# Optimization experiments

Hardware: AMD Instinct MI355X
Metric: run time of the kernel (lower is better)

Reference implementation:

```python
import jax, jax.numpy as jnp
import numpy as np

NEG_SLOPE = 0.2


def gat_conv(x, edge_index, W, a_src, a_dst, b, concat):
    """PyG-style GATConv: add self-loops, linear, edge attention, scatter-softmax, scatter-add."""
    N = x.shape[0]
    H, C = a_src.shape
    loop = jnp.arange(N)
    src = jnp.concatenate([edge_index[0], loop])  # source j (messages flow j -> i)
    dst = jnp.concatenate([edge_index[1], loop])  # target i (aggregation node)
    h = (x @ W).reshape(N, H, C)                  # [N,H,C]
    alpha_s = jnp.sum(h * a_src, axis=-1)         # [N,H]
    alpha_d = jnp.sum(h * a_dst, axis=-1)         # [N,H]
    e = jax.nn.leaky_relu(alpha_s[src] + alpha_d[dst], NEG_SLOPE)  # [E,H]
    # numerically stable scatter-softmax over edges grouped by destination node
    m = jax.ops.segment_max(e, dst, num_segments=N)                # [N,H]
    ex = jnp.exp(e - m[dst])
    denom = jax.ops.segment_sum(ex, dst, num_segments=N)           # [N,H]
    alpha = ex / (denom[dst] + 1e-16)                              # [E,H]
    out = jax.ops.segment_sum(h[src] * alpha[:, :, None], dst, num_segments=N)  # [N,H,C]
    out = out.reshape(N, H * C) if concat else out.mean(axis=1)
    return out + b


def setup_inputs() -> dict:
    key = jax.random.key(0)
    ks = jax.random.split(key, 12)
    N, E, F_IN, HID, OUT, HEADS = 100000, 1600000, 128, 128, 64, 4
    C1 = HID // HEADS
    x = jax.random.normal(ks[0], (N, F_IN), dtype=jnp.float32)
    edge_index = jax.random.randint(ks[1], (2, E), 0, N, dtype=jnp.int64)
    s = 0.05
    return {
        "x": x,
        "edge_index": edge_index,
        "W1": jax.random.normal(ks[2], (F_IN, HEADS * C1), dtype=jnp.float32) * s,
        "a_src1": jax.random.normal(ks[3], (HEADS, C1), dtype=jnp.float32) * s,
        "a_dst1": jax.random.normal(ks[4], (HEADS, C1), dtype=jnp.float32) * s,
        "b1": jnp.zeros((HEADS * C1,), dtype=jnp.float32),
        "W2": jax.random.normal(ks[5], (HID, OUT), dtype=jnp.float32) * s,
        "a_src2": jax.random.normal(ks[6], (1, OUT), dtype=jnp.float32) * s,
        "a_dst2": jax.random.normal(ks[7], (1, OUT), dtype=jnp.float32) * s,
        "b2": jnp.zeros((OUT,), dtype=jnp.float32),
    }


def reference(x, edge_index, W1, a_src1, a_dst1, b1, W2, a_src2, a_dst2, b2):
    h = jax.nn.elu(gat_conv(x, edge_index, W1, a_src1, a_dst1, b1, concat=True))
    # F.dropout(p=0.5, training=False) is the identity in eval mode
    out = gat_conv(h, edge_index, W2, a_src2, a_dst2, b2, concat=False)
    return out
```

## Files before the change

kernel.cpp:

```cpp
#include <hip/hip_runtime.h>
#include <hip/hip_fp16.h>
#include <math.h>
#include <string.h>


#define BSH 9
#define DPB 512
#define NBK 256
#define CH1 16384
#define LOG2E 1.44269504088896f

__device__ __forceinline__ float exp2_fast(float x) {
#if __has_builtin(__builtin_amdgcn_exp2f)
    return __builtin_amdgcn_exp2f(x);
#else
    return exp2f(x);
#endif
}


__global__ __launch_bounds__(256) void bucket_hist(const int* __restrict__ ei, int E, int N,
                                                   unsigned* __restrict__ bcount) {
    __shared__ unsigned hist[NBK];
    int t = threadIdx.x;
    hist[t] = 0;
    __syncthreads();
    int Etot = E + N;
    for (int k = blockIdx.x * 256 + t; k < Etot; k += gridDim.x * 256) {
        int d = (k < E) ? ei[E + k] : (k - E);
        atomicAdd(&hist[d >> BSH], 1u);
    }
    __syncthreads();
    unsigned c = hist[t];
    if (c) atomicAdd(&bcount[t], c);
}

__global__ void scan_buckets(const unsigned* __restrict__ bcount, unsigned* __restrict__ bbase,
                             unsigned* __restrict__ bcursor) {
    __shared__ unsigned s[NBK];
    int t = threadIdx.x;
    unsigned v = bcount[t];
    s[t] = v;
    __syncthreads();
    for (int o = 1; o < NBK; o <<= 1) {
        unsigned add = (t >= o) ? s[t - o] : 0;
        __syncthreads();
        s[t] += add;
        __syncthreads();
    }
    unsigned excl = s[t] - v;
    bbase[t] = excl;
    bcursor[t] = excl;
    if (t == NBK - 1) bbase[NBK] = excl + v;
}

__global__ __launch_bounds__(256) void bucket_scatter(const int* __restrict__ ei, int E, int N,
                                                      unsigned* __restrict__ bcursor,
                                                      unsigned* __restrict__ rec) {
    __shared__ unsigned hist[NBK];
    __shared__ unsigned base[NBK];
    int t = threadIdx.x;
    hist[t] = 0;
    __syncthreads();
    int Etot = E + N;
    int k0 = blockIdx.x * CH1;
    int k1 = min(k0 + CH1, Etot);
    for (int k = k0 + t; k < k1; k += 256) {
        int d = (k < E) ? ei[E + k] : (k - E);
        atomicAdd(&hist[d >> BSH], 1u);
    }
    __syncthreads();
    unsigned c = hist[t];
    base[t] = c ? atomicAdd(&bcursor[t], c) : 0u;
    hist[t] = 0;
    __syncthreads();
    for (int k = k0 + t; k < k1; k += 256) {
        int s, d;
        if (k < E) { s = ei[k]; d = ei[E + k]; } else { s = d = k - E; }
        int b = d >> BSH;
        unsigned r = atomicAdd(&hist[b], 1u);
        rec[base[b] + r] = (unsigned)s | ((unsigned)(d & (DPB - 1)) << 17);
    }
}

__global__ __launch_bounds__(256) void bucket_sort(const unsigned* __restrict__ rec,
                                                   const unsigned* __restrict__ bbase,
                                                   int* __restrict__ offs, int* __restrict__ srcs,
                                                   int N, int Etot) {
    __shared__ unsigned hist[DPB];
    __shared__ unsigned tsum[256];
    int t = threadIdx.x, bb = blockIdx.x;
    unsigned r0 = bbase[bb], r1 = bbase[bb + 1];
    hist[t] = 0;
    hist[t + 256] = 0;
    __syncthreads();
    int dlo = bb << BSH;
    for (unsigned k = r0 + t; k < r1; k += 256) {
        unsigned e = rec[k];
        atomicAdd(&hist[e >> 17], 1u);
    }
    __syncthreads();
    unsigned h0 = hist[2 * t], h1 = hist[2 * t + 1];
    tsum[t] = h0 + h1;
    __syncthreads();
    for (int o = 1; o < 256; o <<= 1) {
        unsigned a = (t >= o) ? tsum[t - o] : 0;
        __syncthreads();
        tsum[t] += a;
        __syncthreads();
    }
    unsigned tb = tsum[t] - (h0 + h1);
    int d0 = dlo + 2 * t;
    if (d0 < N) offs[d0] = (int)(r0 + tb);
    if (d0 + 1 < N) offs[d0 + 1] = (int)(r0 + tb + h0);
    hist[2 * t] = tb;
    hist[2 * t + 1] = tb + h0;
    __syncthreads();
    for (unsigned k = r0 + t; k < r1; k += 256) {
        unsigned e = rec[k];
        unsigned r = atomicAdd(&hist[e >> 17], 1u);
        srcs[r0 + r] = (int)(e & 0x1FFFFu);
    }
    if (bb == 0 && t == 0) offs[N] = Etot;
}


template <int NC, int H, typename InT, typename OutT>
__global__ __launch_bounds__(256) void gemm_k128(const InT* __restrict__ A,
                                                 const float* __restrict__ B,
                                                 OutT* __restrict__ C,
                                                 const float* __restrict__ a_src,
                                                 const float* __restrict__ a_dst,
                                                 float* __restrict__ as,
                                                 float* __restrict__ ad, int M) {
    constexpr int BM = 64, BK = 32, K = 128;
    constexpr int TPR = NC / 4;
    constexpr int R = BM / (256 / TPR);
    constexpr int TXH = TPR / H;
    __shared__ float AsT[BK][BM + 4];
    __shared__ float Bs[BK][NC];
    int tid = threadIdx.x;
    int tx = tid % TPR, ty = tid / TPR;
    int rowBase = blockIdx.x * BM;
    float acc[R][4] = {};
    for (int k0 = 0; k0 < K; k0 += BK) {
#pragma unroll
        for (int i = 0; i < 4; ++i) {
            int lin = tid + i * 256;
            int row = lin >> 4;
            int kp = lin & 15;
            int grow = rowBase + row;
            if (grow >= M) grow = M - 1;
            float2 v;
            if constexpr (sizeof(InT) == 2) {
                __half2 hv = *reinterpret_cast<const __half2*>((const __half*)A + (size_t)grow * K + k0 + kp * 2);
                v = __half22float2(hv);
            } else {
                v = *reinterpret_cast<const float2*>((const float*)A + (size_t)grow * K + k0 + kp * 2);
            }
            AsT[kp * 2][row] = v.x;
            AsT[kp * 2 + 1][row] = v.y;
        }
#pragma unroll
        for (int i = 0; i < (BK * NC) / 1024; ++i) {
            int lin = tid + i * 256;
            int row = lin / (NC / 4);
            int col4 = lin % (NC / 4);
            float4 v = *reinterpret_cast<const float4*>(B + (size_t)(k0 + row) * NC + col4 * 4);
            *reinterpret_cast<float4*>(&Bs[row][col4 * 4]) = v;
        }
        __syncthreads();
#pragma unroll
        for (int kk = 0; kk < BK; ++kk) {
            float4 bv = *reinterpret_cast<const float4*>(&Bs[kk][tx * 4]);
            float a[R];
#pragma unroll
            for (int r4 = 0; r4 < R; r4 += 4) {
                float4 av = *reinterpret_cast<const float4*>(&AsT[kk][ty * R + r4]);
                a[r4] = av.x; a[r4 + 1] = av.y; a[r4 + 2] = av.z; a[r4 + 3] = av.w;
            }
#pragma unroll
            for (int r = 0; r < R; ++r) {
                acc[r][0] = fmaf(a[r], bv.x, acc[r][0]);
                acc[r][1] = fmaf(a[r], bv.y, acc[r][1]);
                acc[r][2] = fmaf(a[r], bv.z, acc[r][2]);
                acc[r][3] = fmaf(a[r], bv.w, acc[r][3]);
            }
        }
        __syncthreads();
    }
    float4 asv = *reinterpret_cast<const float4*>(a_src + tx * 4);
    float4 adv = *reinterpret_cast<const float4*>(a_dst + tx * 4);
#pragma unroll
    for (int r = 0; r < R; ++r) {
        int grow = rowBase + ty * R + r;
        bool live = grow < M;
        if (live) {
            if constexpr (sizeof(OutT) == 2) {
                __half2 p0 = __floats2half2_rn(acc[r][0], acc[r][1]);
                __half2 p1 = __floats2half2_rn(acc[r][2], acc[r][3]);
                __half2* cp = reinterpret_cast<__half2*>((__half*)C + (size_t)grow * NC + tx * 4);
                cp[0] = p0;
                cp[1] = p1;
            } else {
                float4 v = make_float4(acc[r][0], acc[r][1], acc[r][2], acc[r][3]);
                *reinterpret_cast<float4*>((float*)C + (size_t)grow * NC + tx * 4) = v;
            }
        }
        float ps = acc[r][0] * asv.x + acc[r][1] * asv.y + acc[r][2] * asv.z + acc[r][3] * asv.w;
        float pd = acc[r][0] * adv.x + acc[r][1] * adv.y + acc[r][2] * adv.z + acc[r][3] * adv.w;
#pragma unroll
        for (int o = 1; o < TXH; o <<= 1) {
            ps += __shfl_xor(ps, o, 64);
            pd += __shfl_xor(pd, o, 64);
        }
        if ((tx & (TXH - 1)) == 0 && live) {
            int head = tx / TXH;
            as[(size_t)grow * H + head] = ps * LOG2E;
            ad[(size_t)grow * H + head] = pd * LOG2E;
        }
    }
}


template <int H, int ROWS, int COFF, int CW, bool DOELU, typename OutT>
__global__ __launch_bounds__(256) void aggregateQ(const __half* __restrict__ h,
                                                  const float* __restrict__ as,
                                                  const float* __restrict__ ad,
                                                  const int* __restrict__ offs,
                                                  const int* __restrict__ srcs,
                                                  const float* __restrict__ bias,
                                                  OutT* __restrict__ out, int N) {
    constexpr int CPL = CW / 16;
    constexpr int NH2 = CPL / 2;
    unsigned wave = (blockIdx.x * blockDim.x + threadIdx.x) >> 6;
    unsigned lane = threadIdx.x & 63;
    unsigned lig = lane & 15;
    unsigned node = wave * 4u + (lane >> 4);
    bool live = node < (unsigned)N;
    unsigned nc = live ? node : (unsigned)(N - 1);
    unsigned chan = COFF + lig * CPL;
    unsigned head = (chan * H) / ROWS;
    float adv = ad[nc * H + head];
    int e0 = offs[nc], e1 = offs[nc + 1];
    int deg = e1 - e0, e1m1 = e1 - 1;
    int md = deg;
    md = max(md, __shfl_xor(md, 16, 64));
    md = max(md, __shfl_xor(md, 32, 64));
    float2 acc[NH2] = {};
    float den = 0.f;
    for (int k = 0; k < md; k += 2) {
        unsigned ja = (unsigned)srcs[min(e0 + k, e1m1)];
        unsigned jb = (unsigned)srcs[min(e0 + k + 1, e1m1)];
        float ta = as[ja * H + head] + adv;
        float tb = as[jb * H + head] + adv;
        __half2 ha[NH2], hb[NH2];
        if constexpr (NH2 == 4) {
            uint4 va = *reinterpret_cast<const uint4*>(h + ja * (unsigned)ROWS + chan);
            uint4 vb = *reinterpret_cast<const uint4*>(h + jb * (unsigned)ROWS + chan);
            memcpy(ha, &va, 16);
            memcpy(hb, &vb, 16);
        } else {
            uint2 va = *reinterpret_cast<const uint2*>(h + ja * (unsigned)ROWS + chan);
            uint2 vb = *reinterpret_cast<const uint2*>(h + jb * (unsigned)ROWS + chan);
            memcpy(ha, &va, 8);
            memcpy(hb, &vb, 8);
        }
        float xa = exp2_fast(fmaxf(ta, 0.2f * ta));
        float xb = exp2_fast(fmaxf(tb, 0.2f * tb));
        xa = (k < deg) ? xa : 0.f;
        xb = (k + 1 < deg) ? xb : 0.f;
#pragma unroll
        for (int q = 0; q < NH2; ++q) {
            float2 fa = __half22float2(ha[q]);
            float2 fb = __half22float2(hb[q]);
            acc[q].x = fmaf(xa, fa.x, acc[q].x);
            acc[q].y = fmaf(xa, fa.y, acc[q].y);
            acc[q].x = fmaf(xb, fb.x, acc[q].x);
            acc[q].y = fmaf(xb, fb.y, acc[q].y);
        }
        den += xa + xb;
    }
    float r = 1.0f / (den + 1e-16f);
    if (!live) return;
    const float* bp = bias + chan;
    if constexpr (sizeof(OutT) == 2) {
        __half2 st[NH2];
#pragma unroll
        for (int q = 0; q < NH2; ++q) {
            float v0 = acc[q].x * r + bp[2 * q];
            float v1 = acc[q].y * r + bp[2 * q + 1];
            if constexpr (DOELU) {
                v0 = (v0 > 0.f) ? v0 : expm1f(v0);
                v1 = (v1 > 0.f) ? v1 : expm1f(v1);
            }
            st[q] = __floats2half2_rn(v0, v1);
        }
        if constexpr (NH2 == 4) {
            uint4 v; memcpy(&v, st, 16);
            *reinterpret_cast<uint4*>((__half*)out + node * (unsigned)ROWS + chan) = v;
        } else {
            uint2 v; memcpy(&v, st, 8);
            *reinterpret_cast<uint2*>((__half*)out + node * (unsigned)ROWS + chan) = v;
        }
    } else {
        float vs[CPL];
#pragma unroll
        for (int q = 0; q < NH2; ++q) {
            float v0 = acc[q].x * r + bp[2 * q];
            float v1 = acc[q].y * r + bp[2 * q + 1];
            if constexpr (DOELU) {
                v0 = (v0 > 0.f) ? v0 : expm1f(v0);
                v1 = (v1 > 0.f) ? v1 : expm1f(v1);
            }
            vs[2 * q] = v0;
            vs[2 * q + 1] = v1;
        }
#pragma unroll
        for (int q4 = 0; q4 < CPL; q4 += 4) {
            float4 v = make_float4(vs[q4], vs[q4 + 1], vs[q4 + 2], vs[q4 + 3]);
            *reinterpret_cast<float4*>((float*)out + node * (unsigned)ROWS + chan + q4) = v;
        }
    }
}


extern "C" void kernel_launch(void* const* d_in, const int* in_sizes, int n_in,
                              void* d_out, int out_size, void* d_ws, size_t ws_size,
                              hipStream_t stream) {
    const float* x      = (const float*)d_in[0];
    const int*   ei     = (const int*)d_in[1];
    const float* W1     = (const float*)d_in[2];
    const float* a_src1 = (const float*)d_in[3];
    const float* a_dst1 = (const float*)d_in[4];
    const float* b1     = (const float*)d_in[5];
    const float* W2     = (const float*)d_in[6];
    const float* a_src2 = (const float*)d_in[7];
    const float* a_dst2 = (const float*)d_in[8];
    const float* b2     = (const float*)d_in[9];
    float* out = (float*)d_out;

    const int N = out_size / 64;
    const int E = in_sizes[1] / 2;
    const int Etot = E + N;

    size_t off = 0;
    auto carve = [&](size_t bytes) -> void* {
        void* p = (char*)d_ws + off;
        off += (bytes + 255) & ~(size_t)255;
        return p;
    };
    __half* h1      = (__half*)carve((size_t)N * 128 * 2);
    __half* hmid    = (__half*)carve((size_t)N * 128 * 2);
    float* as1      = (float*)carve((size_t)N * 4 * 4);
    float* ad1      = (float*)carve((size_t)N * 4 * 4);
    float* as2      = (float*)carve((size_t)N * 4);
    float* ad2      = (float*)carve((size_t)N * 4);
    int*   offs     = (int*)carve((size_t)(N + 1) * 4);
    int*   srcs     = (int*)carve((size_t)Etot * 4);
    unsigned* rec   = (unsigned*)carve((size_t)Etot * 4);
    unsigned* bcount  = (unsigned*)carve(NBK * 4);
    unsigned* bbase   = (unsigned*)carve((NBK + 1) * 4);
    unsigned* bcursor = (unsigned*)carve(NBK * 4);
    __half* h2      = h1;

    hipMemsetAsync(bcount, 0, NBK * sizeof(unsigned), stream);
    bucket_hist<<<128, 256, 0, stream>>>(ei, E, N, bcount);
    scan_buckets<<<1, 256, 0, stream>>>(bcount, bbase, bcursor);
    bucket_scatter<<<(Etot + CH1 - 1) / CH1, 256, 0, stream>>>(ei, E, N, bcursor, rec);
    bucket_sort<<<(N + DPB - 1) / DPB, 256, 0, stream>>>(rec, bbase, offs, srcs, N, Etot);

    gemm_k128<128, 4, float, __half><<<(N + 63) / 64, 256, 0, stream>>>(
        x, W1, h1, a_src1, a_dst1, as1, ad1, N);
    aggregateQ<4, 128, 0, 64, true, __half><<<(N + 15) / 16, 256, 0, stream>>>(
        h1, as1, ad1, offs, srcs, b1, hmid, N);
    aggregateQ<4, 128, 64, 64, true, __half><<<(N + 15) / 16, 256, 0, stream>>>(
        h1, as1, ad1, offs, srcs, b1, hmid, N);

    gemm_k128<64, 1, __half, __half><<<(N + 63) / 64, 256, 0, stream>>>(
        hmid, W2, h2, a_src2, a_dst2, as2, ad2, N);
    aggregateQ<1, 64, 0, 64, false, float><<<(N + 15) / 16, 256, 0, stream>>>(
        h2, as2, ad2, offs, srcs, b2, out, N);
}
```

Before: 416.0 us.

## Use MFMA f16 matrix cores for GEMMs and merge split layer-1 aggregation

Replaces the scalar-FMA shared-memory GEMM with a kernel built on mfma_f32_16x16x32_f16. The weights are first transposed and cast to half, and the attention projections are computed from the accumulator fragments with lane shuffles. It also merges the two half-channel layer-1 aggregation launches into one launch covering all 128 channels. Inputs and weights now enter the GEMM as fp16, which lowers precision compared with the fp32 FMA path. The per-element stores of C are scattered 2-byte writes, which may cost bandwidth.

```diff
diff --git a/kernel.cpp b/kernel.cpp
--- a/kernel.cpp
+++ b/kernel.cpp
@@ -9,6 +9,9 @@
 #define NBK 256
 #define CH1 16384
 #define LOG2E 1.44269504088896f
+
+using half8 = __attribute__((ext_vector_type(8))) _Float16;
+using floatx4 = __attribute__((ext_vector_type(4))) float;
 
 __device__ __forceinline__ float exp2_fast(float x) {
 #if __has_builtin(__builtin_amdgcn_exp2f)
@@ -125,105 +128,93 @@
 }
 
 
-template <int NC, int H, typename InT, typename OutT>
-__global__ __launch_bounds__(256) void gemm_k128(const InT* __restrict__ A,
-                                                 const float* __restrict__ B,
-                                                 OutT* __restrict__ C,
+__global__ void transpose_w(const float* __restrict__ W, __half* __restrict__ Wt,
+                            int K, int Nc) {
+    int idx = blockIdx.x * 256 + threadIdx.x;
+    if (idx >= K * Nc) return;
+    int n = idx / K, k = idx - n * K;
+    Wt[n * K + k] = __float2half(W[k * Nc + n]);
+}
+
+
+template <int NC, int H, typename InT>
+__global__ __launch_bounds__(256) void gemm_mfma(const InT* __restrict__ A,
+                                                 const __half* __restrict__ Wt,
+                                                 __half* __restrict__ C,
                                                  const float* __restrict__ a_src,
                                                  const float* __restrict__ a_dst,
                                                  float* __restrict__ as,
                                                  float* __restrict__ ad, int M) {
-    constexpr int BM = 64, BK = 32, K = 128;
-    constexpr int TPR = NC / 4;
-    constexpr int R = BM / (256 / TPR);
-    constexpr int TXH = TPR / H;
-    __shared__ float AsT[BK][BM + 4];
-    __shared__ float Bs[BK][NC];
-    int tid = threadIdx.x;
-    int tx = tid % TPR, ty = tid / TPR;
-    int rowBase = blockIdx.x * BM;
-    float acc[R][4] = {};
-    for (int k0 = 0; k0 < K; k0 += BK) {
-#pragma unroll
-        for (int i = 0; i < 4; ++i) {
-            int lin = tid + i * 256;
-            int row = lin >> 4;
-            int kp = lin & 15;
-            int grow = rowBase + row;
-            if (grow >= M) grow = M - 1;
-            float2 v;
-            if constexpr (sizeof(InT) == 2) {
-                __half2 hv = *reinterpret_cast<const __half2*>((const __half*)A + (size_t)grow * K + k0 + kp * 2);
-                v = __half22float2(hv);
-            } else {
-                v = *reinterpret_cast<const float2*>((const float*)A + (size_t)grow * K + k0 + kp * 2);
-            }
-            AsT[kp * 2][row] = v.x;
-            AsT[kp * 2 + 1][row] = v.y;
-        }
-#pragma unroll
-        for (int i = 0; i < (BK * NC) / 1024; ++i) {
-            int lin = tid + i * 256;
-            int row = lin / (NC / 4);
-            int col4 = lin % (NC / 4);
-            float4 v = *reinterpret_cast<const float4*>(B + (size_t)(k0 + row) * NC + col4 * 4);
-            *reinterpret_cast<float4*>(&Bs[row][col4 * 4]) = v;
-        }
-        __syncthreads();
-#pragma unroll
-        for (int kk = 0; kk < BK; ++kk) {
-            float4 bv = *reinterpret_cast<const float4*>(&Bs[kk][tx * 4]);
-            float a[R];
-#pragma unroll
-            for (int r4 = 0; r4 < R; r4 += 4) {
-                float4 av = *reinterpret_cast<const float4*>(&AsT[kk][ty * R + r4]);
-                a[r4] = av.x; a[r4 + 1] = av.y; a[r4 + 2] = av.z; a[r4 + 3] = av.w;
-            }
-#pragma unroll
-            for (int r = 0; r < R; ++r) {
-                acc[r][0] = fmaf(a[r], bv.x, acc[r][0]);
-                acc[r][1] = fmaf(a[r], bv.y, acc[r][1]);
-                acc[r][2] = fmaf(a[r], bv.z, acc[r][2]);
-                acc[r][3] = fmaf(a[r], bv.w, acc[r][3]);
-            }
-        }
-        __syncthreads();
-    }
-    float4 asv = *reinterpret_cast<const float4*>(a_src + tx * 4);
-    float4 adv = *reinterpret_cast<const float4*>(a_dst + tx * 4);
-#pragma unroll
-    for (int r = 0; r < R; ++r) {
-        int grow = rowBase + ty * R + r;
-        bool live = grow < M;
+    constexpr int NT = NC / 16;
+    constexpr int TPH = NT / H;
+    int wave = threadIdx.x >> 6;
+    int lane = threadIdx.x & 63;
+    int quad = lane >> 4, col = lane & 15;
+    int row0 = blockIdx.x * 64 + wave * 16;
+    int arow = row0 + col;
+    if (arow >= M) arow = M - 1;
+    floatx4 acc[NT] = {};
+    const __half* wp = Wt + col * 128 + quad * 8;
+#pragma unroll
+    for (int k0 = 0; k0 < 128; k0 += 32) {
+        half8 af;
+        if constexpr (sizeof(InT) == 4) {
+            const float* ap = (const float*)A + (size_t)arow * 128 + k0 + quad * 8;
+            float4 v0 = *reinterpret_cast<const float4*>(ap);
+            float4 v1 = *reinterpret_cast<const float4*>(ap + 4);
+            af[0] = (_Float16)v0.x; af[1] = (_Float16)v0.y;
+            af[2] = (_Float16)v0.z; af[3] = (_Float16)v0.w;
+            af[4] = (_Float16)v1.x; af[5] = (_Float16)v1.y;
+            af[6] = (_Float16)v1.z; af[7] = (_Float16)v1.w;
+        } else {
+            af = *reinterpret_cast<const half8*>((const __half*)A + (size_t)arow * 128 + k0 + quad * 8);
+        }
+#pragma unroll
+        for (int t = 0; t < NT; ++t) {
+            half8 bf = *reinterpret_cast<const half8*>(wp + t * 16 * 128 + k0);
+            acc[t] = __builtin_amdgcn_mfma_f32_16x16x32_f16(af, bf, acc[t], 0, 0, 0);
+        }
+    }
+    float sa[NT], da[NT];
+#pragma unroll
+    for (int t = 0; t < NT; ++t) {
+        sa[t] = a_src[t * 16 + col];
+        da[t] = a_dst[t * 16 + col];
+    }
+    int rbase = row0 + quad * 4;
+#pragma unroll
+    for (int reg = 0; reg < 4; ++reg) {
+        int row = rbase + reg;
+        bool live = row < M;
         if (live) {
-            if constexpr (sizeof(OutT) == 2) {
-                __half2 p0 = __floats2half2_rn(acc[r][0], acc[r][1]);
-                __half2 p1 = __floats2half2_rn(acc[r][2], acc[r][3]);
-                __half2* cp = reinterpret_cast<__half2*>((__half*)C + (size_t)grow * NC + tx * 4);
-                cp[0] = p0;
-                cp[1] = p1;
-            } else {
-                float4 v = make_float4(acc[r][0], acc[r][1], acc[r][2], acc[r][3]);
-                *reinterpret_cast<float4*>((float*)C + (size_t)grow * NC + tx * 4) = v;
-            }
-        }
-        float ps = acc[r][0] * asv.x + acc[r][1] * asv.y + acc[r][2] * asv.z + acc[r][3] * asv.w;
-        float pd = acc[r][0] * adv.x + acc[r][1] * adv.y + acc[r][2] * adv.z + acc[r][3] * adv.w;
-#pragma unroll
-        for (int o = 1; o < TXH; o <<= 1) {
-            ps += __shfl_xor(ps, o, 64);
-            pd += __shfl_xor(pd, o, 64);
-        }
-        if ((tx & (TXH - 1)) == 0 && live) {
-            int head = tx / TXH;
-            as[(size_t)grow * H + head] = ps * LOG2E;
-            ad[(size_t)grow * H + head] = pd * LOG2E;
-        }
-    }
-}
-
-
-template <int H, int ROWS, int COFF, int CW, bool DOELU, typename OutT>
+#pragma unroll
+            for (int t = 0; t < NT; ++t)
+                C[(size_t)row * NC + t * 16 + col] = __float2half(acc[t][reg]);
+        }
+#pragma unroll
+        for (int h = 0; h < H; ++h) {
+            float ps = 0.f, pd = 0.f;
+#pragma unroll
+            for (int tt = 0; tt < TPH; ++tt) {
+                int t = h * TPH + tt;
+                ps = fmaf(acc[t][reg], sa[t], ps);
+                pd = fmaf(acc[t][reg], da[t], pd);
+            }
+#pragma unroll
+            for (int o = 1; o < 16; o <<= 1) {
+                ps += __shfl_xor(ps, o, 64);
+                pd += __shfl_xor(pd, o, 64);
+            }
+            if (col == 0 && live) {
+                as[(size_t)row * H + h] = ps * LOG2E;
+                ad[(size_t)row * H + h] = pd * LOG2E;
+            }
+        }
+    }
+}
+
+
+template <int H, int ROWS, int CW, bool DOELU, typename OutT>
 __global__ __launch_bounds__(256) void aggregateQ(const __half* __restrict__ h,
                                                   const float* __restrict__ as,
                                                   const float* __restrict__ ad,
@@ -239,7 +230,7 @@
     unsigned node = wave * 4u + (lane >> 4);
     bool live = node < (unsigned)N;
     unsigned nc = live ? node : (unsigned)(N - 1);
-    unsigned chan = COFF + lig * CPL;
+    unsigned chan = lig * CPL;
     unsigned head = (chan * H) / ROWS;
     float adv = ad[nc * H + head];
     int e0 = offs[nc], e1 = offs[nc + 1];
@@ -362,6 +353,8 @@
     unsigned* bcount  = (unsigned*)carve(NBK * 4);
     unsigned* bbase   = (unsigned*)carve((NBK + 1) * 4);
     unsigned* bcursor = (unsigned*)carve(NBK * 4);
+    __half* Wt1h    = (__half*)carve(128 * 128 * 2);
+    __half* Wt2h    = (__half*)carve(64 * 128 * 2);
     __half* h2      = h1;
 
     hipMemsetAsync(bcount, 0, NBK * sizeof(unsigned), stream);
@@ -370,15 +363,16 @@
     bucket_scatter<<<(Etot + CH1 - 1) / CH1, 256, 0, stream>>>(ei, E, N, bcursor, rec);
     bucket_sort<<<(N + DPB - 1) / DPB, 256, 0, stream>>>(rec, bbase, offs, srcs, N, Etot);
 
-    gemm_k128<128, 4, float, __half><<<(N + 63) / 64, 256, 0, stream>>>(
-        x, W1, h1, a_src1, a_dst1, as1, ad1, N);
-    aggregateQ<4, 128, 0, 64, true, __half><<<(N + 15) / 16, 256, 0, stream>>>(
+    transpose_w<<<64, 256, 0, stream>>>(W1, Wt1h, 128, 128);
+    transpose_w<<<32, 256, 0, stream>>>(W2, Wt2h, 128, 64);
+
+    gemm_mfma<128, 4, float><<<(N + 63) / 64, 256, 0, stream>>>(
+        x, Wt1h, h1, a_src1, a_dst1, as1, ad1, N);
+    aggregateQ<4, 128, 128, true, __half><<<(N + 15) / 16, 256, 0, stream>>>(
         h1, as1, ad1, offs, srcs, b1, hmid, N);
-    aggregateQ<4, 128, 64, 64, true, __half><<<(N + 15) / 16, 256, 0, stream>>>(
-        h1, as1, ad1, offs, srcs, b1, hmid, N);
-
-    gemm_k128<64, 1, __half, __half><<<(N + 63) / 64, 256, 0, stream>>>(
-        hmid, W2, h2, a_src2, a_dst2, as2, ad2, N);
-    aggregateQ<1, 64, 0, 64, false, float><<<(N + 15) / 16, 256, 0, stream>>>(
+
+    gemm_mfma<64, 1, __half><<<(N + 63) / 64, 256, 0, stream>>>(
+        hmid, Wt2h, h2, a_src2, a_dst2, as2, ad2, N);
+    aggregateQ<1, 64, 64, false, float><<<(N + 15) / 16, 256, 0, stream>>>(
         h2, as2, ad2, offs, srcs, b2, out, N);
 }
```

New measurement: 383.9 us. 1.08x faster.
